# Kernel optimization log

Measured on AMD Instinct MI355X. Metric: run time of the kernel, lower is better.

The kernel has to match this reference:

```python
import jax, jax.numpy as jnp
import numpy as np

ANNOT = 512
HID = 64
N_STEPS = 8
N_NODES = 100000
N_EDGES = 1600000
NUM_GRAPHS = 64


def setup_inputs() -> dict:
    key = jax.random.key(0)
    ks = jax.random.split(key, 16)
    s = 0.05
    x = jax.random.normal(ks[0], (N_NODES, ANNOT), dtype=jnp.float32)
    edge_index = jax.random.randint(ks[1], (2, N_EDGES), 0, N_NODES, dtype=jnp.int64)
    batch = jnp.sort(jax.random.randint(ks[2], (N_NODES,), 0, NUM_GRAPHS, dtype=jnp.int64))
    return {
        "x": x,
        "edge_index": edge_index,
        "batch": batch,
        "reduce_w": jax.random.normal(ks[3], (ANNOT, HID), dtype=jnp.float32) * s,
        "reduce_b": jnp.zeros((HID,), dtype=jnp.float32),
        "ggc_weight": jax.random.normal(ks[4], (N_STEPS, HID, HID), dtype=jnp.float32) * s,
        "gru_w_ih": jax.random.normal(ks[5], (3 * HID, HID), dtype=jnp.float32) * s,
        "gru_w_hh": jax.random.normal(ks[6], (3 * HID, HID), dtype=jnp.float32) * s,
        "gru_b_ih": jnp.zeros((3 * HID,), dtype=jnp.float32),
        "gru_b_hh": jnp.zeros((3 * HID,), dtype=jnp.float32),
        "gate_w": jax.random.normal(ks[7], (HID, 1), dtype=jnp.float32) * s,
        "gate_b": jnp.zeros((1,), dtype=jnp.float32),
        "out_w": jax.random.normal(ks[8], (HID, 2), dtype=jnp.float32) * s,
        "out_b": jnp.zeros((2,), dtype=jnp.float32),
    }


def _gru_cell(m, h, w_ih, w_hh, b_ih, b_hh):
    gi = m @ w_ih.T + b_ih  # [N, 3H]
    gh = h @ w_hh.T + b_hh
    i_r, i_z, i_n = jnp.split(gi, 3, axis=-1)
    h_r, h_z, h_n = jnp.split(gh, 3, axis=-1)
    r = jax.nn.sigmoid(i_r + h_r)
    z = jax.nn.sigmoid(i_z + h_z)
    n = jnp.tanh(i_n + r * h_n)
    return (1.0 - z) * n + z * h


def _segment_softmax(logits, seg, num_segments):
    # logits: [N, 1]; per-graph softmax (PyG softmax with 1e-16 eps)
    m = jax.ops.segment_max(logits, seg, num_segments=num_segments)
    e = jnp.exp(logits - m[seg])
    s = jax.ops.segment_sum(e, seg, num_segments=num_segments)
    return e / (s[seg] + 1e-16)


def reference(x, edge_index, batch, reduce_w, reduce_b, ggc_weight,
              gru_w_ih, gru_w_hh, gru_b_ih, gru_b_hh,
              gate_w, gate_b, out_w, out_b):
    n_nodes = x.shape[0]
    src, dst = edge_index[0], edge_index[1]

    # reduce: annotation -> hidden
    h = x @ reduce_w + reduce_b  # [N, H]

    # GatedGraphConv: n_steps of (linear -> gather -> scatter-add -> GRU)
    def step(h, W):
        m = h @ W  # [N, H]
        aggr = jax.ops.segment_sum(m[src], dst, num_segments=n_nodes)  # scatter-add
        h_new = _gru_cell(aggr, h, gru_w_ih, gru_w_hh, gru_b_ih, gru_b_hh)
        return h_new, None

    h, _ = jax.lax.scan(step, h, ggc_weight)

    # GlobalAttention pooling: gate_nn -> per-graph softmax; nn -> features
    gate = _segment_softmax(h @ gate_w + gate_b, batch, NUM_GRAPHS)  # [N, 1]
    feat = h @ out_w + out_b  # [N, 2]
    pooled = jax.ops.segment_sum(gate * feat, batch, num_segments=NUM_GRAPHS)  # [G, 2]

    return jax.nn.softmax(pooled, axis=1)
```

## Files before the change

kernel.cpp:

```cpp
#include <hip/hip_runtime.h>
#include <math.h>

#define HID 64
#define ANNOT 512
#define NSTEPS 8
#define PCHUNK 4096
#define CSR_CAP 10240

typedef __attribute__((ext_vector_type(8))) short short8_t;
typedef __attribute__((ext_vector_type(16))) float floatx16;

__device__ __forceinline__ float sigmoidf_(float x) { return 1.0f / (1.0f + __expf(-x)); }

__device__ __forceinline__ float bf2f(unsigned short u) {
  return __uint_as_float(((unsigned)u) << 16);
}
__device__ __forceinline__ unsigned short f2bf(float f) {
  unsigned u = __float_as_uint(f);
  unsigned r = ((u >> 16) & 1u) + 0x7fffu;
  return (unsigned short)((u + r) >> 16);
}
__device__ __forceinline__ float bflo(unsigned u) { return __uint_as_float(u << 16); }
__device__ __forceinline__ float bfhi(unsigned u) { return __uint_as_float(u & 0xffff0000u); }
__device__ __forceinline__ unsigned cvtpk_bf16(float lo, float hi) {
  unsigned r;
  asm("v_cvt_pk_bf16_f32 %0, %1, %2" : "=v"(r) : "v"(lo), "v"(hi));
  return r;
}

__global__ void k_wpack(const float* __restrict__ Wr, unsigned short* __restrict__ Wpack) {
  const int t = blockIdx.x;
  const int kc = t >> 1, nt = t & 1;
  const int l = threadIdx.x;
  const int c = nt * 32 + (l & 31);
  unsigned short* dst = Wpack + ((size_t)t * 64 + l) * 8;
#pragma unroll
  for (int j = 0; j < 8; ++j) {
    int k = kc * 16 + (l >> 5) * 8 + j;
    dst[j] = f2bf(Wr[(size_t)k * HID + c]);
  }
}

__global__ __launch_bounds__(256) void k_reduce(
    const float* __restrict__ x, const unsigned short* __restrict__ Wpack,
    const float* __restrict__ br, unsigned short* __restrict__ h, int n_nodes)
{
  const int wave = threadIdx.x >> 6;
  const int lane = threadIdx.x & 63;
  const int hi = lane >> 5;
  const int l31 = lane & 31;
  const int rbase = blockIdx.x * 128 + wave * 32;
  const int arow = rbase + l31;
  const bool avalid = arow < n_nodes;
  const float* xrow = x + (size_t)arow * ANNOT + hi * 8;

  floatx16 acc[2];
#pragma unroll
  for (int nt = 0; nt < 2; ++nt)
#pragma unroll
    for (int j = 0; j < 16; ++j) acc[nt][j] = 0.f;

#pragma unroll 4
  for (int kc = 0; kc < 32; ++kc) {
    short8_t a = {0, 0, 0, 0, 0, 0, 0, 0};
    if (avalid) {
      float4 u0 = *(const float4*)(xrow + kc * 16);
      float4 u1 = *(const float4*)(xrow + kc * 16 + 4);
      int4 ai;
      ai.x = (int)cvtpk_bf16(u0.x, u0.y);
      ai.y = (int)cvtpk_bf16(u0.z, u0.w);
      ai.z = (int)cvtpk_bf16(u1.x, u1.y);
      ai.w = (int)cvtpk_bf16(u1.z, u1.w);
      a = *(short8_t*)&ai;
    }
    const short8_t* Bb = (const short8_t*)(Wpack + (size_t)kc * 2 * 64 * 8);
#pragma unroll
    for (int nt = 0; nt < 2; ++nt) {
      short8_t b = Bb[nt * 64 + lane];
      acc[nt] = __builtin_amdgcn_mfma_f32_32x32x16_bf16(a, b, acc[nt], 0, 0, 0);
    }
  }

  float bias[2];
  bias[0] = br[l31];
  bias[1] = br[32 + l31];
#pragma unroll
  for (int reg = 0; reg < 16; ++reg) {
    int row = rbase + (reg & 3) + 8 * (reg >> 2) + 4 * hi;
    if (row < n_nodes) {
#pragma unroll
      for (int nt = 0; nt < 2; ++nt) {
        float v = acc[nt][reg] + bias[nt];
        h[(size_t)row * HID + nt * 32 + l31] = f2bf(v);
      }
    }
  }
}

__global__ void k_bbig(const float* __restrict__ ggc_w, const float* __restrict__ w_ih,
                       const float* __restrict__ w_hh, unsigned short* __restrict__ Bpack)
{
  const int nt = blockIdx.x;
  const int kc = blockIdx.y;
  const int s  = blockIdx.z;
  const int l  = threadIdx.x;
  const int c = nt * 32 + (l & 31);
  const int sec = c >> 6, f = c & 63;
  unsigned short outv[8];
#pragma unroll
  for (int j = 0; j < 8; ++j) {
    int k = kc * 16 + (l >> 5) * 8 + j;
    float v = 0.f;
    if (k < 64) {
      if (sec < 3) {
        const float* Ws = ggc_w + ((size_t)s * 64 + k) * 64;
        const float* wr = w_ih + (size_t)(sec * 64 + f) * 64;
        float a = 0.f;
        for (int q = 0; q < 64; ++q) a += Ws[q] * wr[q];
        v = a;
      }
    } else {
      int k2 = k - 64;
      if (sec == 0)      v = w_hh[(size_t)f * 64 + k2];
      else if (sec == 1) v = w_hh[(size_t)(64 + f) * 64 + k2];
      else if (sec == 3) v = w_hh[(size_t)(128 + f) * 64 + k2];
    }
    outv[j] = f2bf(v);
  }
  unsigned short* dst = Bpack + ((((size_t)s * 8 + kc) * 8 + nt) * 64 + l) * 8;
#pragma unroll
  for (int j = 0; j < 8; ++j) dst[j] = outv[j];
}

__global__ __launch_bounds__(256) void k_pcnt(const int* __restrict__ dstv, int E,
                                              int* __restrict__ bukCnt, int nbuk)
{
  __shared__ int lh[256];
  lh[threadIdx.x] = 0;
  __syncthreads();
  for (int e = blockIdx.x * blockDim.x + threadIdx.x; e < E; e += gridDim.x * blockDim.x)
    atomicAdd(&lh[dstv[e] >> 9], 1);
  __syncthreads();
  if (threadIdx.x < nbuk) {
    int v = lh[threadIdx.x];
    if (v) atomicAdd(&bukCnt[threadIdx.x], v);
  }
}

__global__ void k_bscan(const int* __restrict__ bukCnt, int nbuk,
                        int* __restrict__ bukBase, int* __restrict__ bukCur,
                        int* __restrict__ row_ptr, int n_nodes, int E)
{
  if (threadIdx.x == 0 && blockIdx.x == 0) {
    int run = 0;
    for (int b = 0; b < nbuk; ++b) { bukBase[b] = run; bukCur[b] = run; run += bukCnt[b]; }
    bukBase[nbuk] = run;
    row_ptr[n_nodes] = E;
  }
}

__global__ __launch_bounds__(256) void k_part(
    const int* __restrict__ srcv, const int* __restrict__ dstv, int E,
    int* __restrict__ bukCur, unsigned* __restrict__ rec, int nbuk)
{
  __shared__ int lhist[256], lexcl[256], lbase[256], lcur[256];
  __shared__ unsigned lrec[PCHUNK];
  __shared__ unsigned char lbuk[PCHUNK];
  const int t = threadIdx.x;
  const int nchunk = (E + PCHUNK - 1) / PCHUNK;
  for (int c = blockIdx.x; c < nchunk; c += gridDim.x) {
    const int e0 = c * PCHUNK;
    const int cnt = min(PCHUNK, E - e0);
    lhist[t] = 0;
    __syncthreads();
    int myS[16], myD[16];
#pragma unroll
    for (int i = 0; i < 16; ++i) {
      int j = t + i * 256;
      myS[i] = -1; myD[i] = 0;
      if (j < cnt) {
        int e = e0 + j;
        myS[i] = srcv[e];
        myD[i] = dstv[e];
        atomicAdd(&lhist[myD[i] >> 9], 1);
      }
    }
    __syncthreads();
    int v = lhist[t];
    lexcl[t] = v;
    __syncthreads();
    for (int d = 1; d < 256; d <<= 1) {
      int u = (t >= d) ? lexcl[t - d] : 0;
      __syncthreads();
      lexcl[t] += u;
      __syncthreads();
    }
    int excl = lexcl[t] - v;
    __syncthreads();
    lexcl[t] = excl;
    lcur[t] = excl;
    if (v > 0) lbase[t] = atomicAdd(&bukCur[t], v);
    __syncthreads();
#pragma unroll
    for (int i = 0; i < 16; ++i) {
      if (myS[i] >= 0) {
        int b = myD[i] >> 9;
        int p = atomicAdd(&lcur[b], 1);
        lrec[p] = (unsigned)myS[i] | ((unsigned)(myD[i] & 511) << 23);
        lbuk[p] = (unsigned char)b;
      }
    }
    __syncthreads();
    for (int j = t; j < cnt; j += 256) {
      int b = lbuk[j];
      rec[(size_t)lbase[b] + (j - lexcl[b])] = lrec[j];
    }
    __syncthreads();
  }
}

__global__ __launch_bounds__(512) void k_csr(
    const unsigned* __restrict__ rec, const int* __restrict__ bukBase,
    int* __restrict__ row_ptr, int* __restrict__ csr_src, int n_nodes)
{
  __shared__ int cnt[512], off[512], cur[512];
  __shared__ int outbuf[CSR_CAP];
  const int b = blockIdx.x;
  const int t = threadIdx.x;
  const int beg = bukBase[b], end = bukBase[b + 1];
  const int m = end - beg;
  const int node0 = b << 9;
  cnt[t] = 0;
  __syncthreads();
  for (int j = t; j < m; j += 512)
    atomicAdd(&cnt[rec[beg + j] >> 23], 1);
  __syncthreads();
  int v = cnt[t];
  off[t] = v;
  __syncthreads();
  for (int d = 1; d < 512; d <<= 1) {
    int u = (t >= d) ? off[t - d] : 0;
    __syncthreads();
    off[t] += u;
    __syncthreads();
  }
  int excl = off[t] - v;
  cur[t] = excl;
  int node = node0 + t;
  if (node < n_nodes) row_ptr[node] = beg + excl;
  __syncthreads();
  for (int j = t; j < m; j += 512) {
    unsigned r = rec[beg + j];
    int p = atomicAdd(&cur[r >> 23], 1);
    if (p < CSR_CAP) outbuf[p] = (int)(r & 0x7FFFFFu);
  }
  __syncthreads();
  for (int j = t; j < m; j += 512)
    csr_src[beg + j] = (j < CSR_CAP) ? outbuf[j] : 0;
}

__global__ __launch_bounds__(256) void k_aggr(
    const uint4* __restrict__ h16, const int* __restrict__ row_ptr,
    const int* __restrict__ csr_src, uint4* __restrict__ aggr16, int n_nodes)
{
  const int wid = threadIdx.x >> 6;
  const int lane = threadIdx.x & 63;
  const int grp = lane >> 3;
  const int l8 = lane & 7;
  const int n = blockIdx.x * 32 + wid * 8 + grp;
  const bool valid = n < n_nodes;
  const int nc = valid ? n : (n_nodes - 1);
  const int beg = row_ptr[nc];
  const int end = valid ? row_ptr[nc + 1] : beg;
  const int last = end - 1;
  float a0 = 0.f, a1 = 0.f, a2 = 0.f, a3 = 0.f, a4 = 0.f, a5 = 0.f, a6 = 0.f, a7 = 0.f;

  for (int e = beg; e < end; e += 4) {
    int s0 = csr_src[min(e,     last)]; if (e     > last) s0 = n_nodes;
    int s1 = csr_src[min(e + 1, last)]; if (e + 1 > last) s1 = n_nodes;
    int s2 = csr_src[min(e + 2, last)]; if (e + 2 > last) s2 = n_nodes;
    int s3 = csr_src[min(e + 3, last)]; if (e + 3 > last) s3 = n_nodes;
    uint4 v0 = h16[(size_t)s0 * 8 + l8];
    uint4 v1 = h16[(size_t)s1 * 8 + l8];
    uint4 v2 = h16[(size_t)s2 * 8 + l8];
    uint4 v3 = h16[(size_t)s3 * 8 + l8];
    a0 += bflo(v0.x) + bflo(v1.x) + bflo(v2.x) + bflo(v3.x);
    a1 += bfhi(v0.x) + bfhi(v1.x) + bfhi(v2.x) + bfhi(v3.x);
    a2 += bflo(v0.y) + bflo(v1.y) + bflo(v2.y) + bflo(v3.y);
    a3 += bfhi(v0.y) + bfhi(v1.y) + bfhi(v2.y) + bfhi(v3.y);
    a4 += bflo(v0.z) + bflo(v1.z) + bflo(v2.z) + bflo(v3.z);
    a5 += bfhi(v0.z) + bfhi(v1.z) + bfhi(v2.z) + bfhi(v3.z);
    a6 += bflo(v0.w) + bflo(v1.w) + bflo(v2.w) + bflo(v3.w);
    a7 += bfhi(v0.w) + bfhi(v1.w) + bfhi(v2.w) + bfhi(v3.w);
  }

  if (valid) {
    uint4 o;
    o.x = cvtpk_bf16(a0, a1);
    o.y = cvtpk_bf16(a2, a3);
    o.z = cvtpk_bf16(a4, a5);
    o.w = cvtpk_bf16(a6, a7);
    aggr16[(size_t)n * 8 + l8] = o;
  }
}

__global__ __launch_bounds__(256) void k_gru(
    const unsigned short* __restrict__ aggr, unsigned short* __restrict__ h,
    const unsigned short* __restrict__ Bpack_s,
    const float* __restrict__ b_ih, const float* __restrict__ b_hh, int n_nodes)
{
  const int wave = threadIdx.x >> 6;
  const int lane = threadIdx.x & 63;
  const int hi = lane >> 5;
  const int l31 = lane & 31;
  const int rbase = blockIdx.x * 128 + wave * 32;
  const int arow = rbase + l31;
  const bool avalid = arow < n_nodes;

  floatx16 acc[8];
#pragma unroll
  for (int nt = 0; nt < 8; ++nt)
#pragma unroll
    for (int j = 0; j < 16; ++j) acc[nt][j] = 0.f;

#pragma unroll
  for (int kc = 0; kc < 8; ++kc) {
    const unsigned short* Asrc = (kc < 4) ? aggr : h;
    short8_t a = {0, 0, 0, 0, 0, 0, 0, 0};
    if (avalid)
      a = *(const short8_t*)(Asrc + (size_t)arow * HID + (kc & 3) * 16 + hi * 8);
    const short8_t* Bb = (const short8_t*)(Bpack_s + (size_t)kc * 8 * 64 * 8);
#pragma unroll
    for (int nt = 0; nt < 8; ++nt) {
      short8_t b = Bb[nt * 64 + lane];
      acc[nt] = __builtin_amdgcn_mfma_f32_32x32x16_bf16(a, b, acc[nt], 0, 0, 0);
    }
  }

  float bi[2][3], bh[2][3];
#pragma unroll
  for (int half = 0; half < 2; ++half) {
    int f = half * 32 + l31;
    bi[half][0] = b_ih[f]; bi[half][1] = b_ih[64 + f]; bi[half][2] = b_ih[128 + f];
    bh[half][0] = b_hh[f]; bh[half][1] = b_hh[64 + f]; bh[half][2] = b_hh[128 + f];
  }
#pragma unroll
  for (int reg = 0; reg < 16; ++reg) {
    int row = rbase + (reg & 3) + 8 * (reg >> 2) + 4 * hi;
    if (row < n_nodes) {
#pragma unroll
      for (int half = 0; half < 2; ++half) {
        int f = half * 32 + l31;
        float rg = sigmoidf_(acc[half][reg] + bi[half][0] + bh[half][0]);
        float zg = sigmoidf_(acc[2 + half][reg] + bi[half][1] + bh[half][1]);
        float ng = tanhf(acc[4 + half][reg] + bi[half][2] + rg * (acc[6 + half][reg] + bh[half][2]));
        size_t idx = (size_t)row * HID + f;
        float hold = bf2f(h[idx]);
        h[idx] = f2bf((1.f - zg) * ng + zg * hold);
      }
    }
  }
}

__global__ __launch_bounds__(256) void k_pool(
    const unsigned short* __restrict__ h, const int* __restrict__ batch,
    const float* __restrict__ gate_w, const float* __restrict__ gate_b,
    const float* __restrict__ out_w, const float* __restrict__ out_b,
    float* __restrict__ acc3, int n_nodes)
{
  __shared__ float sacc[192];
  int t = threadIdx.x;
  if (t < 192) sacc[t] = 0.f;
  __syncthreads();
  int n = blockIdx.x * blockDim.x + t;
  if (n < n_nodes) {
    float g = gate_b[0], f0 = out_b[0], f1 = out_b[1];
    const ushort4* hr = (const ushort4*)(h + (size_t)n * HID);
#pragma unroll
    for (int q = 0; q < 16; ++q) {
      ushort4 v = hr[q];
      float h0 = bf2f(v.x), h1 = bf2f(v.y), h2 = bf2f(v.z), h3 = bf2f(v.w);
      int k = q * 4;
      g += h0 * gate_w[k] + h1 * gate_w[k + 1] + h2 * gate_w[k + 2] + h3 * gate_w[k + 3];
      f0 += h0 * out_w[2 * k] + h1 * out_w[2 * k + 2] + h2 * out_w[2 * k + 4] + h3 * out_w[2 * k + 6];
      f1 += h0 * out_w[2 * k + 1] + h1 * out_w[2 * k + 3] + h2 * out_w[2 * k + 5] + h3 * out_w[2 * k + 7];
    }
    float e = expf(g);
    int b = batch[n];
    atomicAdd(&sacc[3 * b + 0], e);
    atomicAdd(&sacc[3 * b + 1], e * f0);
    atomicAdd(&sacc[3 * b + 2], e * f1);
  }
  __syncthreads();
  if (t < 192) {
    float v = sacc[t];
    if (v != 0.f) atomicAdd(&acc3[t], v);
  }
}

__global__ void k_pool3(const float* __restrict__ acc3, float* __restrict__ out, int n_graphs) {
  int g = blockIdx.x * blockDim.x + threadIdx.x;
  if (g < n_graphs) {
    float s = acc3[3 * g] + 1e-16f;
    float p0 = acc3[3 * g + 1] / s, p1 = acc3[3 * g + 2] / s;
    float m = fmaxf(p0, p1);
    float e0 = expf(p0 - m), e1 = expf(p1 - m);
    float d = e0 + e1;
    out[2 * g] = e0 / d;
    out[2 * g + 1] = e1 / d;
  }
}

extern "C" void kernel_launch(void* const* d_in, const int* in_sizes, int n_in,
                              void* d_out, int out_size, void* d_ws, size_t ws_size,
                              hipStream_t stream)
{
  const float* x        = (const float*)d_in[0];
  const int*   edge     = (const int*)d_in[1];
  const int*   batch    = (const int*)d_in[2];
  const float* reduce_w = (const float*)d_in[3];
  const float* reduce_b = (const float*)d_in[4];
  const float* ggc_w    = (const float*)d_in[5];
  const float* w_ih     = (const float*)d_in[6];
  const float* w_hh     = (const float*)d_in[7];
  const float* b_ih     = (const float*)d_in[8];
  const float* b_hh     = (const float*)d_in[9];
  const float* gate_w   = (const float*)d_in[10];
  const float* gate_b   = (const float*)d_in[11];
  const float* out_w    = (const float*)d_in[12];
  const float* out_b    = (const float*)d_in[13];
  float* out = (float*)d_out;

  const int n_nodes  = in_sizes[0] / ANNOT;
  const int E        = in_sizes[1] / 2;
  const int n_graphs = out_size / 2;
  const int* src  = edge;
  const int* dstv = edge + E;
  const int nbuk = (n_nodes + 511) >> 9;

  size_t off = 0;
  auto alloc = [&](size_t bytes) { size_t o = off; off = (off + bytes + 255) & ~(size_t)255; return o; };
  char* w = (char*)d_ws;

  unsigned short* h    = (unsigned short*)(w + alloc((size_t)(n_nodes + 1) * HID * 2));
  unsigned short* aggr = (unsigned short*)(w + alloc((size_t)n_nodes * HID * 2));
  int*   csr_src = (int*)(w + alloc((size_t)E * 4));
  int*   row_ptr = (int*)(w + alloc((size_t)(n_nodes + 1) * 4));
  unsigned* rec  = (unsigned*)(w + alloc((size_t)E * 4));
  int*   bukCnt  = (int*)(w + alloc((size_t)(nbuk + 1) * 4));
  int*   bukBase = (int*)(w + alloc((size_t)(nbuk + 1) * 4));
  int*   bukCur  = (int*)(w + alloc((size_t)(nbuk + 1) * 4));
  unsigned short* Bpack = (unsigned short*)(w + alloc((size_t)NSTEPS * 8 * 8 * 64 * 8 * 2));
  unsigned short* Wpack = (unsigned short*)(w + alloc((size_t)64 * 64 * 8 * 2));
  float* acc3    = (float*)(w + alloc(192 * 4));
  (void)ws_size; (void)n_in;

  hipMemsetAsync(bukCnt, 0, (size_t)(nbuk + 1) * 4, stream);
  hipMemsetAsync(acc3, 0, 192 * 4, stream);
  hipMemsetAsync(h + (size_t)n_nodes * HID, 0, HID * 2, stream);

  const int gN256 = (n_nodes + 255) / 256;
  const int nchunk = (E + PCHUNK - 1) / PCHUNK;

  k_wpack<<<64, 64, 0, stream>>>(reduce_w, Wpack);
  k_reduce<<<(n_nodes + 127) / 128, 256, 0, stream>>>(x, Wpack, reduce_b, h, n_nodes);
  k_bbig<<<dim3(8, 8, NSTEPS), 64, 0, stream>>>(ggc_w, w_ih, w_hh, Bpack);

  k_pcnt<<<1024, 256, 0, stream>>>(dstv, E, bukCnt, nbuk);
  k_bscan<<<1, 1, 0, stream>>>(bukCnt, nbuk, bukBase, bukCur, row_ptr, n_nodes, E);
  k_part<<<nchunk, 256, 0, stream>>>(src, dstv, E, bukCur, rec, nbuk);
  k_csr<<<nbuk, 512, 0, stream>>>(rec, bukBase, row_ptr, csr_src, n_nodes);

  for (int s = 0; s < NSTEPS; ++s) {
    k_aggr<<<(n_nodes + 31) / 32, 256, 0, stream>>>((const uint4*)h, row_ptr, csr_src, (uint4*)aggr, n_nodes);
    k_gru<<<(n_nodes + 127) / 128, 256, 0, stream>>>(aggr, h, Bpack + (size_t)s * 8 * 8 * 64 * 8, b_ih, b_hh, n_nodes);
  }

  k_pool<<<gN256, 256, 0, stream>>>(h, batch, gate_w, gate_b, out_w, out_b, acc3, n_nodes);
  k_pool3<<<1, 64, 0, stream>>>(acc3, out, n_graphs);
}
```

Before: 652.9 us.

## Fuse edge aggregation into GRU kernel via LDS staging with ping-pong hidden buffers

Merges the per-step gather/sum aggregation kernel and the MFMA GRU kernel into one launch. Aggregated rows are written to a swizzled shared-memory buffer instead of global memory, and the hidden state now ping-pongs between two buffers so that concurrent blocks never read rows that are being overwritten. This removes the global write and read of the aggr array and halves the launches per step. In exchange each thread now handles 4 nodes sequentially in the gather phase, which lowers memory-level parallelism, and the GRU phase has to wait for the slowest node in its block.

```diff
diff --git a/kernel.cpp b/kernel.cpp
--- a/kernel.cpp
+++ b/kernel.cpp
@@ -259,62 +259,65 @@
     csr_src[beg + j] = (j < CSR_CAP) ? outbuf[j] : 0;
 }
 
-__global__ __launch_bounds__(256) void k_aggr(
-    const uint4* __restrict__ h16, const int* __restrict__ row_ptr,
-    const int* __restrict__ csr_src, uint4* __restrict__ aggr16, int n_nodes)
-{
-  const int wid = threadIdx.x >> 6;
-  const int lane = threadIdx.x & 63;
-  const int grp = lane >> 3;
-  const int l8 = lane & 7;
-  const int n = blockIdx.x * 32 + wid * 8 + grp;
-  const bool valid = n < n_nodes;
-  const int nc = valid ? n : (n_nodes - 1);
-  const int beg = row_ptr[nc];
-  const int end = valid ? row_ptr[nc + 1] : beg;
-  const int last = end - 1;
-  float a0 = 0.f, a1 = 0.f, a2 = 0.f, a3 = 0.f, a4 = 0.f, a5 = 0.f, a6 = 0.f, a7 = 0.f;
-
-  for (int e = beg; e < end; e += 4) {
-    int s0 = csr_src[min(e,     last)]; if (e     > last) s0 = n_nodes;
-    int s1 = csr_src[min(e + 1, last)]; if (e + 1 > last) s1 = n_nodes;
-    int s2 = csr_src[min(e + 2, last)]; if (e + 2 > last) s2 = n_nodes;
-    int s3 = csr_src[min(e + 3, last)]; if (e + 3 > last) s3 = n_nodes;
-    uint4 v0 = h16[(size_t)s0 * 8 + l8];
-    uint4 v1 = h16[(size_t)s1 * 8 + l8];
-    uint4 v2 = h16[(size_t)s2 * 8 + l8];
-    uint4 v3 = h16[(size_t)s3 * 8 + l8];
-    a0 += bflo(v0.x) + bflo(v1.x) + bflo(v2.x) + bflo(v3.x);
-    a1 += bfhi(v0.x) + bfhi(v1.x) + bfhi(v2.x) + bfhi(v3.x);
-    a2 += bflo(v0.y) + bflo(v1.y) + bflo(v2.y) + bflo(v3.y);
-    a3 += bfhi(v0.y) + bfhi(v1.y) + bfhi(v2.y) + bfhi(v3.y);
-    a4 += bflo(v0.z) + bflo(v1.z) + bflo(v2.z) + bflo(v3.z);
-    a5 += bfhi(v0.z) + bfhi(v1.z) + bfhi(v2.z) + bfhi(v3.z);
-    a6 += bflo(v0.w) + bflo(v1.w) + bflo(v2.w) + bflo(v3.w);
-    a7 += bfhi(v0.w) + bfhi(v1.w) + bfhi(v2.w) + bfhi(v3.w);
-  }
-
-  if (valid) {
-    uint4 o;
-    o.x = cvtpk_bf16(a0, a1);
-    o.y = cvtpk_bf16(a2, a3);
-    o.z = cvtpk_bf16(a4, a5);
-    o.w = cvtpk_bf16(a6, a7);
-    aggr16[(size_t)n * 8 + l8] = o;
-  }
-}
-
-__global__ __launch_bounds__(256) void k_gru(
-    const unsigned short* __restrict__ aggr, unsigned short* __restrict__ h,
+__global__ __launch_bounds__(256) void k_fused(
+    const uint4* __restrict__ h16_in, const unsigned short* __restrict__ h_in,
+    unsigned short* __restrict__ h_out,
+    const int* __restrict__ row_ptr, const int* __restrict__ csr_src,
     const unsigned short* __restrict__ Bpack_s,
     const float* __restrict__ b_ih, const float* __restrict__ b_hh, int n_nodes)
 {
-  const int wave = threadIdx.x >> 6;
-  const int lane = threadIdx.x & 63;
+  __shared__ uint4 albuf[128 * 8];
+  const int tid = threadIdx.x;
+  const int rbase = blockIdx.x * 128;
+
+  {
+    const int g32 = tid >> 3;
+    const int l8 = tid & 7;
+#pragma unroll
+    for (int i = 0; i < 4; ++i) {
+      const int rl = g32 * 4 + i;
+      const int n = rbase + rl;
+      const bool valid = n < n_nodes;
+      const int nc = valid ? n : (n_nodes - 1);
+      const int beg = row_ptr[nc];
+      const int end = valid ? row_ptr[nc + 1] : beg;
+      const int last = end - 1;
+      float a0 = 0.f, a1 = 0.f, a2 = 0.f, a3 = 0.f, a4 = 0.f, a5 = 0.f, a6 = 0.f, a7 = 0.f;
+
+      for (int e = beg; e < end; e += 4) {
+        int s0 = csr_src[min(e,     last)]; if (e     > last) s0 = n_nodes;
+        int s1 = csr_src[min(e + 1, last)]; if (e + 1 > last) s1 = n_nodes;
+        int s2 = csr_src[min(e + 2, last)]; if (e + 2 > last) s2 = n_nodes;
+        int s3 = csr_src[min(e + 3, last)]; if (e + 3 > last) s3 = n_nodes;
+        uint4 v0 = h16_in[(size_t)s0 * 8 + l8];
+        uint4 v1 = h16_in[(size_t)s1 * 8 + l8];
+        uint4 v2 = h16_in[(size_t)s2 * 8 + l8];
+        uint4 v3 = h16_in[(size_t)s3 * 8 + l8];
+        a0 += bflo(v0.x) + bflo(v1.x) + bflo(v2.x) + bflo(v3.x);
+        a1 += bfhi(v0.x) + bfhi(v1.x) + bfhi(v2.x) + bfhi(v3.x);
+        a2 += bflo(v0.y) + bflo(v1.y) + bflo(v2.y) + bflo(v3.y);
+        a3 += bfhi(v0.y) + bfhi(v1.y) + bfhi(v2.y) + bfhi(v3.y);
+        a4 += bflo(v0.z) + bflo(v1.z) + bflo(v2.z) + bflo(v3.z);
+        a5 += bfhi(v0.z) + bfhi(v1.z) + bfhi(v2.z) + bfhi(v3.z);
+        a6 += bflo(v0.w) + bflo(v1.w) + bflo(v2.w) + bflo(v3.w);
+        a7 += bfhi(v0.w) + bfhi(v1.w) + bfhi(v2.w) + bfhi(v3.w);
+      }
+      uint4 o;
+      o.x = cvtpk_bf16(a0, a1);
+      o.y = cvtpk_bf16(a2, a3);
+      o.z = cvtpk_bf16(a4, a5);
+      o.w = cvtpk_bf16(a6, a7);
+      albuf[rl * 8 + (l8 ^ (rl & 7))] = o;
+    }
+  }
+  __syncthreads();
+
+  const int wave = tid >> 6;
+  const int lane = tid & 63;
   const int hi = lane >> 5;
   const int l31 = lane & 31;
-  const int rbase = blockIdx.x * 128 + wave * 32;
-  const int arow = rbase + l31;
+  const int rl = wave * 32 + l31;
+  const int arow = rbase + rl;
   const bool avalid = arow < n_nodes;
 
   floatx16 acc[8];
@@ -325,10 +328,17 @@
 
 #pragma unroll
   for (int kc = 0; kc < 8; ++kc) {
-    const unsigned short* Asrc = (kc < 4) ? aggr : h;
-    short8_t a = {0, 0, 0, 0, 0, 0, 0, 0};
-    if (avalid)
-      a = *(const short8_t*)(Asrc + (size_t)arow * HID + (kc & 3) * 16 + hi * 8);
+    short8_t a;
+    if (kc < 4) {
+      int slot = kc * 2 + hi;
+      uint4 v = albuf[rl * 8 + (slot ^ (rl & 7))];
+      a = *(short8_t*)&v;
+    } else {
+      short8_t az = {0, 0, 0, 0, 0, 0, 0, 0};
+      a = az;
+      if (avalid)
+        a = *(const short8_t*)(h_in + (size_t)arow * HID + (kc & 3) * 16 + hi * 8);
+    }
     const short8_t* Bb = (const short8_t*)(Bpack_s + (size_t)kc * 8 * 64 * 8);
 #pragma unroll
     for (int nt = 0; nt < 8; ++nt) {
@@ -346,7 +356,7 @@
   }
 #pragma unroll
   for (int reg = 0; reg < 16; ++reg) {
-    int row = rbase + (reg & 3) + 8 * (reg >> 2) + 4 * hi;
+    int row = rbase + wave * 32 + (reg & 3) + 8 * (reg >> 2) + 4 * hi;
     if (row < n_nodes) {
 #pragma unroll
       for (int half = 0; half < 2; ++half) {
@@ -355,8 +365,8 @@
         float zg = sigmoidf_(acc[2 + half][reg] + bi[half][1] + bh[half][1]);
         float ng = tanhf(acc[4 + half][reg] + bi[half][2] + rg * (acc[6 + half][reg] + bh[half][2]));
         size_t idx = (size_t)row * HID + f;
-        float hold = bf2f(h[idx]);
-        h[idx] = f2bf((1.f - zg) * ng + zg * hold);
+        float hold = bf2f(h_in[idx]);
+        h_out[idx] = f2bf((1.f - zg) * ng + zg * hold);
       }
     }
   }
@@ -442,8 +452,8 @@
   auto alloc = [&](size_t bytes) { size_t o = off; off = (off + bytes + 255) & ~(size_t)255; return o; };
   char* w = (char*)d_ws;
 
-  unsigned short* h    = (unsigned short*)(w + alloc((size_t)(n_nodes + 1) * HID * 2));
-  unsigned short* aggr = (unsigned short*)(w + alloc((size_t)n_nodes * HID * 2));
+  unsigned short* hA   = (unsigned short*)(w + alloc((size_t)(n_nodes + 1) * HID * 2));
+  unsigned short* hB   = (unsigned short*)(w + alloc((size_t)(n_nodes + 1) * HID * 2));
   int*   csr_src = (int*)(w + alloc((size_t)E * 4));
   int*   row_ptr = (int*)(w + alloc((size_t)(n_nodes + 1) * 4));
   unsigned* rec  = (unsigned*)(w + alloc((size_t)E * 4));
@@ -457,13 +467,14 @@
 
   hipMemsetAsync(bukCnt, 0, (size_t)(nbuk + 1) * 4, stream);
   hipMemsetAsync(acc3, 0, 192 * 4, stream);
-  hipMemsetAsync(h + (size_t)n_nodes * HID, 0, HID * 2, stream);
+  hipMemsetAsync(hA + (size_t)n_nodes * HID, 0, HID * 2, stream);
+  hipMemsetAsync(hB + (size_t)n_nodes * HID, 0, HID * 2, stream);
 
   const int gN256 = (n_nodes + 255) / 256;
   const int nchunk = (E + PCHUNK - 1) / PCHUNK;
 
   k_wpack<<<64, 64, 0, stream>>>(reduce_w, Wpack);
-  k_reduce<<<(n_nodes + 127) / 128, 256, 0, stream>>>(x, Wpack, reduce_b, h, n_nodes);
+  k_reduce<<<(n_nodes + 127) / 128, 256, 0, stream>>>(x, Wpack, reduce_b, hA, n_nodes);
   k_bbig<<<dim3(8, 8, NSTEPS), 64, 0, stream>>>(ggc_w, w_ih, w_hh, Bpack);
 
   k_pcnt<<<1024, 256, 0, stream>>>(dstv, E, bukCnt, nbuk);
@@ -471,11 +482,15 @@
   k_part<<<nchunk, 256, 0, stream>>>(src, dstv, E, bukCur, rec, nbuk);
   k_csr<<<nbuk, 512, 0, stream>>>(rec, bukBase, row_ptr, csr_src, n_nodes);
 
+  unsigned short* hin = hA;
+  unsigned short* hout = hB;
   for (int s = 0; s < NSTEPS; ++s) {
-    k_aggr<<<(n_nodes + 31) / 32, 256, 0, stream>>>((const uint4*)h, row_ptr, csr_src, (uint4*)aggr, n_nodes);
-    k_gru<<<(n_nodes + 127) / 128, 256, 0, stream>>>(aggr, h, Bpack + (size_t)s * 8 * 8 * 64 * 8, b_ih, b_hh, n_nodes);
-  }
-
-  k_pool<<<gN256, 256, 0, stream>>>(h, batch, gate_w, gate_b, out_w, out_b, acc3, n_nodes);
+    k_fused<<<(n_nodes + 127) / 128, 256, 0, stream>>>(
+        (const uint4*)hin, hin, hout, row_ptr, csr_src,
+        Bpack + (size_t)s * 8 * 8 * 64 * 8, b_ih, b_hh, n_nodes);
+    unsigned short* tmp = hin; hin = hout; hout = tmp;
+  }
+
+  k_pool<<<gN256, 256, 0, stream>>>(hin, batch, gate_w, gate_b, out_w, out_b, acc3, n_nodes);
   k_pool3<<<1, 64, 0, stream>>>(acc3, out, n_graphs);
 }
```

Result: slower. 744.0 us (+14.0%).
